# Kernel tuning notes

Measured on AMD Instinct MI355X. Metric: run time of the kernel, lower is better.

The kernel has to match this reference:

```python
import jax, jax.numpy as jnp
import numpy as np

B, N, C = 16, 2048, 256
C4 = C // 4
BN_EPS = 1e-5


def setup_inputs() -> dict:
    key = jax.random.key(0)
    ks = jax.random.split(key, 9)
    return {
        "x": jax.random.normal(ks[0], (B, N, C), jnp.float32),
        "Wq": jax.random.normal(ks[1], (C4, C), jnp.float32) * (1.0 / np.sqrt(C)),
        "Wk": jax.random.normal(ks[2], (C4, C), jnp.float32) * (1.0 / np.sqrt(C)),
        "Wv": jax.random.normal(ks[3], (C, C), jnp.float32) * (1.0 / np.sqrt(C)),
        "bv": jax.random.normal(ks[4], (C,), jnp.float32) * 0.01,
        "Wt": jax.random.normal(ks[5], (C, C), jnp.float32) * (1.0 / np.sqrt(C)),
        "bt": jax.random.normal(ks[6], (C,), jnp.float32) * 0.01,
        "gamma": jnp.ones((C,), jnp.float32),
        "beta": jnp.zeros((C,), jnp.float32),
        "bn_mean": jax.random.normal(ks[7], (C,), jnp.float32) * 0.1,
        "bn_var": jax.random.uniform(ks[8], (C,), jnp.float32, 0.5, 1.5),
    }


def reference(x, Wq, Wk, Wv, bv, Wt, bt, gamma, beta, bn_mean, bn_var):
    # x: (B, N, C) -> channel-first (B, C, N) as in the torch module
    xc = jnp.transpose(x, (0, 2, 1))                       # (B, C, N)
    q = jnp.einsum('oc,bcn->bno', Wq, xc)                  # (B, N, C4)
    k = jnp.einsum('oc,bcn->bon', Wk, xc)                  # (B, C4, N)
    # v_conv is computed in the original module but its output is never used;
    # it does not affect the forward output.
    energy = jnp.einsum('bno,bom->bnm', q, k)              # (B, N, N)
    attn = jax.nn.softmax(energy, axis=-1)
    # offset-attention double normalization: divide by column sums
    attn = attn / (1e-6 + jnp.sum(attn, axis=1, keepdims=True))
    x_r = jnp.einsum('bcn,bnm->bcm', xc, attn)             # (B, C, N)
    d = xc - x_r
    t = jnp.einsum('oc,bcn->bon', Wt, d) + bt[None, :, None]
    bn = gamma[None, :, None] * (t - bn_mean[None, :, None]) \
         * jax.lax.rsqrt(bn_var[None, :, None] + BN_EPS) + beta[None, :, None]
    out = xc + jnp.maximum(bn, 0.0)                        # residual + ReLU
    return jnp.transpose(out, (0, 2, 1))                   # (B, N, C)
```

## Files before the change

### kernel.cpp

```cpp
#include <hip/hip_runtime.h>
#include <math.h>
#include <stdint.h>

constexpr int B_ = 16, N_ = 2048, C_ = 256, K_ = 64;
constexpr float EPS_BN = 1e-5f;

typedef __attribute__((ext_vector_type(8))) short short8;
typedef __attribute__((ext_vector_type(16))) float f32x16;

#define MFMA32(A, Bf, Cc) __builtin_amdgcn_mfma_f32_32x32x16_bf16(A, Bf, Cc, 0, 0, 0)

constexpr size_t SZ_QK  = (size_t)B_*N_*K_*2;
constexpr size_t WSB_QH = 0;
constexpr size_t WSB_QL = WSB_QH + SZ_QK;
constexpr size_t WSB_KH = WSB_QL + SZ_QK;
constexpr size_t WSB_KL = WSB_KH + SZ_QK;
constexpr size_t WSB_Z  = WSB_KL + SZ_QK;
constexpr size_t WSB_CS = WSB_Z  + (size_t)B_*N_*4;
constexpr size_t WSB_WQT= WSB_CS + (size_t)B_*N_*4;
constexpr size_t WSB_WKT= WSB_WQT+ (size_t)C_*K_*4;
constexpr size_t WSB_WTT= WSB_WKT+ (size_t)C_*K_*4;
constexpr size_t WSB_S  = WSB_WTT+ (size_t)C_*C_*4;
constexpr size_t WSB_CB = WSB_S  + (size_t)C_*4;
constexpr size_t WSB_O  = (WSB_CB + (size_t)C_*4 + 255) & ~(size_t)255;

constexpr size_t XT_LO = (size_t)B_*N_*C_*2;

__device__ inline unsigned short bf16_rne(float f) {
  uint32_t u = __float_as_uint(f);
  uint32_t r = u + 0x7FFFu + ((u >> 16) & 1u);
  return (unsigned short)(r >> 16);
}

#define GLOAD_LDS16(g, l) __builtin_amdgcn_global_load_lds( \
    (const __attribute__((address_space(1))) unsigned int*)(g), \
    (__attribute__((address_space(3))) unsigned int*)(l), 16, 0, 0)

__global__ void k0_prep(const float* __restrict__ Wq, const float* __restrict__ Wk,
                        const float* __restrict__ Wt, const float* __restrict__ bt,
                        const float* __restrict__ gamma, const float* __restrict__ beta,
                        const float* __restrict__ mean, const float* __restrict__ var,
                        char* __restrict__ ws) {
  int o = blockIdx.x, c = threadIdx.x;
  ((float*)(ws + WSB_WTT))[(size_t)c*C_ + o] = Wt[(size_t)o*C_ + c];
  if (o < K_) {
    ((float*)(ws + WSB_WQT))[(size_t)c*K_ + o] = Wq[(size_t)o*C_ + c];
    ((float*)(ws + WSB_WKT))[(size_t)c*K_ + o] = Wk[(size_t)o*C_ + c];
  }
  if (o == 0) {
    float s = gamma[c] * rsqrtf(var[c] + EPS_BN);
    ((float*)(ws + WSB_S))[c]  = s;
    ((float*)(ws + WSB_CB))[c] = s * (bt[c] - mean[c]) + beta[c];
  }
}

__global__ __launch_bounds__(256) void k1_qk(const float* __restrict__ x,
                                             char* __restrict__ ws,
                                             char* __restrict__ xtbuf) {
  __shared__ float xs[32][260];
  const float* WqT = (const float*)(ws + WSB_WQT);
  const float* WkT = (const float*)(ws + WSB_WKT);
  unsigned short* qh = (unsigned short*)(ws + WSB_QH);
  unsigned short* ql = (unsigned short*)(ws + WSB_QL);
  unsigned short* kh = (unsigned short*)(ws + WSB_KH);
  unsigned short* kl = (unsigned short*)(ws + WSB_KL);
  int b = blockIdx.x >> 6, nt = blockIdx.x & 63;
  int n0 = nt * 32, tid = threadIdx.x;

  const float4* xg = (const float4*)(x + ((size_t)b*N_ + n0)*C_);
#pragma unroll
  for (int i = 0; i < 8; i++) {
    int f = tid + i*256;
    int r = f >> 6, c4 = f & 63;
    *(float4*)&xs[r][c4*4] = xg[f];
  }
  __syncthreads();

  int o = tid & 63, rg = tid >> 6;
  float aq[8], ak[8];
#pragma unroll
  for (int j = 0; j < 8; j++) { aq[j] = 0.f; ak[j] = 0.f; }
  for (int c = 0; c < C_; c++) {
    float wq = WqT[c*K_ + o];
    float wk = WkT[c*K_ + o];
#pragma unroll
    for (int j = 0; j < 8; j++) {
      float xv = xs[rg*8 + j][c];
      aq[j] = fmaf(xv, wq, aq[j]);
      ak[j] = fmaf(xv, wk, ak[j]);
    }
  }
#pragma unroll
  for (int j = 0; j < 8; j++) {
    int n = n0 + rg*8 + j;
    size_t base = ((size_t)b*N_ + n)*K_ + o;
    float q = aq[j];
    uint32_t qb = __float_as_uint(q) & 0xFFFF0000u;
    qh[base] = (unsigned short)(qb >> 16);
    ql[base] = bf16_rne(q - __uint_as_float(qb));
    float k = ak[j];
    uint32_t kb = __float_as_uint(k) & 0xFFFF0000u;
    kh[base] = (unsigned short)(kb >> 16);
    kl[base] = bf16_rne(k - __uint_as_float(kb));
  }
#pragma unroll
  for (int nc = 0; nc < 4; nc++) {
    uint32_t hw[4], lw[4];
#pragma unroll
    for (int jj = 0; jj < 4; jj++) {
      float a  = xs[nc*8 + jj*2    ][tid];
      float bv = xs[nc*8 + jj*2 + 1][tid];
      uint32_t ab = __float_as_uint(a)  & 0xFFFF0000u;
      uint32_t bb = __float_as_uint(bv) & 0xFFFF0000u;
      hw[jj] = (ab >> 16) | bb;
      float alo = a  - __uint_as_float(ab);
      float blo = bv - __uint_as_float(bb);
      lw[jj] = (uint32_t)bf16_rne(alo) | ((uint32_t)bf16_rne(blo) << 16);
    }
    size_t toff = ((size_t)(b*64 + nt))*16384 + ((size_t)nc*256 + tid)*16;
    *(uint4*)(xtbuf + toff)         = make_uint4(hw[0], hw[1], hw[2], hw[3]);
    *(uint4*)(xtbuf + XT_LO + toff) = make_uint4(lw[0], lw[1], lw[2], lw[3]);
  }
}

__global__ __launch_bounds__(256) void k3_stats(char* __restrict__ ws) {
  int b = blockIdx.x >> 4, nb = blockIdx.x & 15;
  int tid = threadIdx.x, wave = tid >> 6, l = tid & 63;
  int lo5 = l & 31, hi5 = l >> 5;
  int n = nb*128 + wave*32 + lo5;

  short8 qhf[4], qlf[4];
  size_t qoff = ((size_t)b*N_ + n)*K_;
#pragma unroll
  for (int cs = 0; cs < 4; cs++) {
    qhf[cs] = *(const short8*)(ws + WSB_QH + (qoff + cs*16 + hi5*8)*2);
    qlf[cs] = *(const short8*)(ws + WSB_QL + (qoff + cs*16 + hi5*8)*2);
  }
  float M = -3.0e38f, S = 0.f;
  for (int mt = 0; mt < 64; mt++) {
    int mm0 = mt*32;
    size_t koff = ((size_t)b*N_ + mm0 + lo5)*K_;
    short8 khf[4], klf[4];
#pragma unroll
    for (int cs = 0; cs < 4; cs++) {
      khf[cs] = *(const short8*)(ws + WSB_KH + (koff + cs*16 + hi5*8)*2);
      klf[cs] = *(const short8*)(ws + WSB_KL + (koff + cs*16 + hi5*8)*2);
    }
    f32x16 E = {0.f};
#pragma unroll
    for (int cs = 0; cs < 4; cs++) {
      E = MFMA32(khf[cs], qhf[cs], E);
      E = MFMA32(khf[cs], qlf[cs], E);
      E = MFMA32(klf[cs], qhf[cs], E);
    }
    float tmax = E[0];
#pragma unroll
    for (int r = 1; r < 16; r++) tmax = fmaxf(tmax, E[r]);
    float nM = fmaxf(M, tmax);
    float sc = __expf(M - nM);
    float ss = 0.f;
#pragma unroll
    for (int r = 0; r < 16; r++) ss += __expf(E[r] - nM);
    S = fmaf(S, sc, ss);
    M = nM;
  }
  float Mo = __shfl_xor(M, 32, 64);
  float So = __shfl_xor(S, 32, 64);
  float Mg = fmaxf(M, Mo);
  float Sg = S*__expf(M - Mg) + So*__expf(Mo - Mg);
  if (hi5 == 0)
    ((float*)(ws + WSB_Z))[(size_t)b*N_ + n] = Mg + __logf(Sg);
}

__global__ __launch_bounds__(256) void k4_ov(char* __restrict__ ws,
                                             const char* __restrict__ xtbuf) {
  __shared__ __align__(16) char xtile[32768];
  __shared__ float zs[32];
  int b = blockIdx.x >> 5, mblk = blockIdx.x & 31;
  int m0 = mblk*64;
  int tid = threadIdx.x, wave = tid >> 6, l = tid & 63;
  int lo5 = l & 31, hi5 = l >> 5;
  int msub = wave >> 1, c0 = (wave & 1)*128;
  int mg = m0 + msub*32 + lo5;

  short8 khf[4], klf[4];
  size_t koff = ((size_t)b*N_ + mg)*K_;
#pragma unroll
  for (int cs = 0; cs < 4; cs++) {
    khf[cs] = *(const short8*)(ws + WSB_KH + (koff + cs*16 + hi5*8)*2);
    klf[cs] = *(const short8*)(ws + WSB_KL + (koff + cs*16 + hi5*8)*2);
  }
  f32x16 accO[4];
#pragma unroll
  for (int ct = 0; ct < 4; ct++) accO[ct] = (f32x16){0.f};
  float csum = 0.f;
  const float* Zp = (const float*)(ws + WSB_Z);

  for (int nt = 0; nt < 64; nt++) {
    int nn0 = nt*32;
    __syncthreads();
    size_t src = (size_t)(b*64 + nt)*16384 + (size_t)tid*16;
#pragma unroll
    for (int i = 0; i < 4; i++)
      GLOAD_LDS16(xtbuf + src + (size_t)i*4096, xtile + tid*16 + i*4096);
#pragma unroll
    for (int i = 0; i < 4; i++)
      GLOAD_LDS16(xtbuf + XT_LO + src + (size_t)i*4096, xtile + 16384 + tid*16 + i*4096);
    if (tid < 32) zs[tid] = Zp[(size_t)b*N_ + nn0 + tid];
    short8 qaf[4], qalf[4];
    size_t qoff = ((size_t)b*N_ + nn0 + lo5)*K_;
#pragma unroll
    for (int cs = 0; cs < 4; cs++) {
      qaf[cs]  = *(const short8*)(ws + WSB_QH + (qoff + cs*16 + hi5*8)*2);
      qalf[cs] = *(const short8*)(ws + WSB_QL + (qoff + cs*16 + hi5*8)*2);
    }
    __syncthreads();
    f32x16 E = {0.f};
#pragma unroll
    for (int cs = 0; cs < 4; cs++) {
      E = MFMA32(qaf[cs],  khf[cs], E);
      E = MFMA32(qaf[cs],  klf[cs], E);
      E = MFMA32(qalf[cs], khf[cs], E);
    }
    float ph[16], pl[16];
#pragma unroll
    for (int r = 0; r < 16; r++) {
      int nr = (r & 3) + 8*(r >> 2) + 4*hi5;
      float p = __expf(E[r] - zs[nr]);
      csum += p;
      uint32_t pb = __float_as_uint(p) & 0xFFFF0000u;
      ph[r] = __uint_as_float(pb);
      pl[r] = p - ph[r];
    }
    uint32_t Wh[8], Wl[8];
#pragma unroll
    for (int i = 0; i < 8; i++) {
      Wh[i] = (__float_as_uint(ph[2*i]) >> 16) | (__float_as_uint(ph[2*i+1]) & 0xFFFF0000u);
      uint32_t w;
      asm("v_cvt_pk_bf16_f32 %0, %1, %2" : "=v"(w) : "v"(pl[2*i]), "v"(pl[2*i+1]));
      Wl[i] = w;
    }
    short8 pha[2], pla[2];
#pragma unroll
    for (int s = 0; s < 2; s++) {
      uint32_t a0 = Wh[s*4+0], b0 = Wh[s*4+2];
      uint32_t a1 = Wh[s*4+1], b1 = Wh[s*4+3];
      asm("v_permlane32_swap_b32 %0, %1" : "+v"(a0), "+v"(b0));
      asm("v_permlane32_swap_b32 %0, %1" : "+v"(a1), "+v"(b1));
      union { uint32_t w[4]; short8 s8; } uh;
      uh.w[0] = a0; uh.w[1] = a1; uh.w[2] = b0; uh.w[3] = b1;
      pha[s] = uh.s8;
      uint32_t c0w = Wl[s*4+0], d0 = Wl[s*4+2];
      uint32_t c1w = Wl[s*4+1], d1 = Wl[s*4+3];
      asm("v_permlane32_swap_b32 %0, %1" : "+v"(c0w), "+v"(d0));
      asm("v_permlane32_swap_b32 %0, %1" : "+v"(c1w), "+v"(d1));
      union { uint32_t w[4]; short8 s8; } ul;
      ul.w[0] = c0w; ul.w[1] = c1w; ul.w[2] = d0; ul.w[3] = d1;
      pla[s] = ul.s8;
    }
#pragma unroll
    for (int ct = 0; ct < 4; ct++) {
      int cc = c0 + ct*32 + lo5;
      short8 bh[2], bl[2];
#pragma unroll
      for (int ns = 0; ns < 2; ns++) {
        size_t off = ((size_t)((ns*2 + hi5)*256 + cc))*16;
        bh[ns] = *(const short8*)(xtile + off);
        bl[ns] = *(const short8*)(xtile + 16384 + off);
      }
#pragma unroll
      for (int ns = 0; ns < 2; ns++) {
        accO[ct] = MFMA32(pha[ns], bh[ns], accO[ct]);
        accO[ct] = MFMA32(pha[ns], bl[ns], accO[ct]);
        accO[ct] = MFMA32(pla[ns], bh[ns], accO[ct]);
      }
    }
  }
  csum += __shfl_xor(csum, 32, 64);
  if ((wave & 1) == 0 && hi5 == 0)
    ((float*)(ws + WSB_CS))[(size_t)b*N_ + mg] = csum;
  float* Op = (float*)(ws + WSB_O);
#pragma unroll
  for (int ct = 0; ct < 4; ct++) {
#pragma unroll
    for (int r = 0; r < 16; r++) {
      int mm = m0 + msub*32 + (r & 3) + 8*(r >> 2) + 4*hi5;
      int cc = c0 + ct*32 + lo5;
      Op[((size_t)b*N_ + mm)*C_ + cc] = accO[ct][r];
    }
  }
}

constexpr int BR5 = 64;
__global__ __launch_bounds__(256) void k5_epi(const float* __restrict__ x,
                                              char* __restrict__ ws,
                                              float* __restrict__ out) {
  const float* WtT  = (const float*)(ws + WSB_WTT);
  const float* Sarr = (const float*)(ws + WSB_S);
  const float* Carr = (const float*)(ws + WSB_CB);
  const float* colsum = (const float*)(ws + WSB_CS);
  const float* Oraw = (const float*)(ws + WSB_O);
  __shared__ float ds[BR5][C_];
  __shared__ float icsL[BR5];
  int b = blockIdx.x >> 5, nt = blockIdx.x & 31;
  int n0 = nt*BR5, tid = threadIdx.x;
  if (tid < BR5) icsL[tid] = 1.0f / (1e-6f + colsum[(size_t)b*N_ + n0 + tid]);
  __syncthreads();
  const float4* xg = (const float4*)(x    + ((size_t)b*N_ + n0)*C_);
  const float4* og = (const float4*)(Oraw + ((size_t)b*N_ + n0)*C_);
#pragma unroll
  for (int i = 0; i < 16; i++) {
    int f = tid + i*256;
    int r = f >> 6;
    float4 xv = xg[f];
    float4 ov = og[f];
    float ic = icsL[r];
    float4 d;
    d.x = xv.x - ov.x*ic; d.y = xv.y - ov.y*ic;
    d.z = xv.z - ov.z*ic; d.w = xv.w - ov.w*ic;
    *(float4*)&ds[r][(f & 63)*4] = d;
  }
  __syncthreads();
  int og_ = tid & 63, rg = tid >> 6;
  float acc[16][4];
#pragma unroll
  for (int r = 0; r < 16; r++)
#pragma unroll
    for (int j = 0; j < 4; j++) acc[r][j] = 0.f;
  for (int cc = 0; cc < C_; cc++) {
    float4 w = *(const float4*)&WtT[(size_t)cc*C_ + og_*4];
#pragma unroll
    for (int r = 0; r < 16; r++) {
      float dv = ds[rg*16 + r][cc];
      acc[r][0] = fmaf(dv, w.x, acc[r][0]);
      acc[r][1] = fmaf(dv, w.y, acc[r][1]);
      acc[r][2] = fmaf(dv, w.z, acc[r][2]);
      acc[r][3] = fmaf(dv, w.w, acc[r][3]);
    }
  }
  float4 s4 = *(const float4*)&Sarr[og_*4];
  float4 c4 = *(const float4*)&Carr[og_*4];
#pragma unroll
  for (int r = 0; r < 16; r++) {
    size_t row = (size_t)b*N_ + n0 + rg*16 + r;
    float4 xv = *(const float4*)&x[row*C_ + og_*4];
    float4 o;
    float bn0 = fmaf(s4.x, acc[r][0], c4.x);
    float bn1 = fmaf(s4.y, acc[r][1], c4.y);
    float bn2 = fmaf(s4.z, acc[r][2], c4.z);
    float bn3 = fmaf(s4.w, acc[r][3], c4.w);
    o.x = xv.x + (bn0 > 0.f ? bn0 : 0.f);
    o.y = xv.y + (bn1 > 0.f ? bn1 : 0.f);
    o.z = xv.z + (bn2 > 0.f ? bn2 : 0.f);
    o.w = xv.w + (bn3 > 0.f ? bn3 : 0.f);
    *(float4*)&out[row*C_ + og_*4] = o;
  }
}

extern "C" void kernel_launch(void* const* d_in, const int* in_sizes, int n_in,
                              void* d_out, int out_size, void* d_ws, size_t ws_size,
                              hipStream_t stream) {
  (void)in_sizes; (void)n_in; (void)out_size; (void)ws_size;
  const float* x     = (const float*)d_in[0];
  const float* Wq    = (const float*)d_in[1];
  const float* Wk    = (const float*)d_in[2];
  const float* Wt    = (const float*)d_in[5];
  const float* bt    = (const float*)d_in[6];
  const float* gamma = (const float*)d_in[7];
  const float* beta  = (const float*)d_in[8];
  const float* mean  = (const float*)d_in[9];
  const float* var   = (const float*)d_in[10];
  char* ws = (char*)d_ws;
  char* xt = (char*)d_out;
  float* out = (float*)d_out;

  k0_prep <<<C_,        C_,  0, stream>>>(Wq, Wk, Wt, bt, gamma, beta, mean, var, ws);
  k1_qk   <<<B_*64,     256, 0, stream>>>(x, ws, xt);
  k3_stats<<<B_*16,     256, 0, stream>>>(ws);
  k4_ov   <<<B_*32,     256, 0, stream>>>(ws, xt);
  k5_epi  <<<B_*32,     256, 0, stream>>>(x, ws, out);
}
```

Baseline: 451.6 us.

## Fuse epilogue transform GEMM into attention kernel with double-buffered LDS staging

Merges the separate epilogue kernel into the attention-output kernel. Each block now normalises its output by the column sums, forms d = x - x_r in a swizzled LDS tile, and runs the Wt projection with split-bf16 MFMA before applying BN, ReLU and the residual. This removes the round trip of the raw O tensor and colsum through global memory, and moves the epilogue from scalar FMA loops onto MFMA. It also double-buffers the x-tile and Q loads across iterations to overlap loads with compute. The trade-off is doubled LDS use (64KB) and more register pressure, which may limit occupancy.

```diff
diff --git a/kernel.cpp b/kernel.cpp
--- a/kernel.cpp
+++ b/kernel.cpp
@@ -16,15 +16,14 @@
 constexpr size_t WSB_KH = WSB_QL + SZ_QK;
 constexpr size_t WSB_KL = WSB_KH + SZ_QK;
 constexpr size_t WSB_Z  = WSB_KL + SZ_QK;
-constexpr size_t WSB_CS = WSB_Z  + (size_t)B_*N_*4;
-constexpr size_t WSB_WQT= WSB_CS + (size_t)B_*N_*4;
+constexpr size_t WSB_WQT= WSB_Z  + (size_t)B_*N_*4;
 constexpr size_t WSB_WKT= WSB_WQT+ (size_t)C_*K_*4;
-constexpr size_t WSB_WTT= WSB_WKT+ (size_t)C_*K_*4;
-constexpr size_t WSB_S  = WSB_WTT+ (size_t)C_*C_*4;
+constexpr size_t WSB_S  = WSB_WKT+ (size_t)C_*K_*4;
 constexpr size_t WSB_CB = WSB_S  + (size_t)C_*4;
-constexpr size_t WSB_O  = (WSB_CB + (size_t)C_*4 + 255) & ~(size_t)255;
-
-constexpr size_t XT_LO = (size_t)B_*N_*C_*2;
+constexpr size_t WSB_WBH= WSB_CB + (size_t)C_*4;
+constexpr size_t WSB_WBL= WSB_WBH+ (size_t)C_*C_*2;
+constexpr size_t WSB_XT = (WSB_WBL + (size_t)C_*C_*2 + 255) & ~(size_t)255;
+constexpr size_t XT_HALF= (size_t)B_*N_*C_*2;
 
 __device__ inline unsigned short bf16_rne(float f) {
   uint32_t u = __float_as_uint(f);
@@ -42,7 +41,12 @@
                         const float* __restrict__ mean, const float* __restrict__ var,
                         char* __restrict__ ws) {
   int o = blockIdx.x, c = threadIdx.x;
-  ((float*)(ws + WSB_WTT))[(size_t)c*C_ + o] = Wt[(size_t)o*C_ + c];
+  {
+    float w = Wt[(size_t)o*C_ + c];
+    uint32_t wb = __float_as_uint(w) & 0xFFFF0000u;
+    ((unsigned short*)(ws + WSB_WBH))[(size_t)o*C_ + c] = (unsigned short)(wb >> 16);
+    ((unsigned short*)(ws + WSB_WBL))[(size_t)o*C_ + c] = bf16_rne(w - __uint_as_float(wb));
+  }
   if (o < K_) {
     ((float*)(ws + WSB_WQT))[(size_t)c*K_ + o] = Wq[(size_t)o*C_ + c];
     ((float*)(ws + WSB_WKT))[(size_t)c*K_ + o] = Wk[(size_t)o*C_ + c];
@@ -118,8 +122,8 @@
       lw[jj] = (uint32_t)bf16_rne(alo) | ((uint32_t)bf16_rne(blo) << 16);
     }
     size_t toff = ((size_t)(b*64 + nt))*16384 + ((size_t)nc*256 + tid)*16;
-    *(uint4*)(xtbuf + toff)         = make_uint4(hw[0], hw[1], hw[2], hw[3]);
-    *(uint4*)(xtbuf + XT_LO + toff) = make_uint4(lw[0], lw[1], lw[2], lw[3]);
+    *(uint4*)(xtbuf + toff)           = make_uint4(hw[0], hw[1], hw[2], hw[3]);
+    *(uint4*)(xtbuf + XT_HALF + toff) = make_uint4(lw[0], lw[1], lw[2], lw[3]);
   }
 }
 
@@ -138,8 +142,7 @@
   }
   float M = -3.0e38f, S = 0.f;
   for (int mt = 0; mt < 64; mt++) {
-    int mm0 = mt*32;
-    size_t koff = ((size_t)b*N_ + mm0 + lo5)*K_;
+    size_t koff = ((size_t)b*N_ + mt*32 + lo5)*K_;
     short8 khf[4], klf[4];
 #pragma unroll
     for (int cs = 0; cs < 4; cs++) {
@@ -172,16 +175,21 @@
     ((float*)(ws + WSB_Z))[(size_t)b*N_ + n] = Mg + __logf(Sg);
 }
 
-__global__ __launch_bounds__(256) void k4_ov(char* __restrict__ ws,
-                                             const char* __restrict__ xtbuf) {
-  __shared__ __align__(16) char xtile[32768];
-  __shared__ float zs[32];
+__global__ __launch_bounds__(256, 2) void k4_ov(const float* __restrict__ x,
+                                                char* __restrict__ ws,
+                                                float* __restrict__ out) {
+  __shared__ __align__(16) char xtile[65536];
+  __shared__ float zsb[2][32];
+  __shared__ float csL[64];
   int b = blockIdx.x >> 5, mblk = blockIdx.x & 31;
   int m0 = mblk*64;
   int tid = threadIdx.x, wave = tid >> 6, l = tid & 63;
   int lo5 = l & 31, hi5 = l >> 5;
   int msub = wave >> 1, c0 = (wave & 1)*128;
   int mg = m0 + msub*32 + lo5;
+  const float* Zp = (const float*)(ws + WSB_Z);
+  const char* XTH = ws + WSB_XT;
+  const char* XTL = ws + WSB_XT + XT_HALF;
 
   short8 khf[4], klf[4];
   size_t koff = ((size_t)b*N_ + mg)*K_;
@@ -194,39 +202,37 @@
 #pragma unroll
   for (int ct = 0; ct < 4; ct++) accO[ct] = (f32x16){0.f};
   float csum = 0.f;
-  const float* Zp = (const float*)(ws + WSB_Z);
-
-  for (int nt = 0; nt < 64; nt++) {
-    int nn0 = nt*32;
-    __syncthreads();
+
+  auto STAGE = [&](int nt, int buf) {
     size_t src = (size_t)(b*64 + nt)*16384 + (size_t)tid*16;
-#pragma unroll
-    for (int i = 0; i < 4; i++)
-      GLOAD_LDS16(xtbuf + src + (size_t)i*4096, xtile + tid*16 + i*4096);
-#pragma unroll
-    for (int i = 0; i < 4; i++)
-      GLOAD_LDS16(xtbuf + XT_LO + src + (size_t)i*4096, xtile + 16384 + tid*16 + i*4096);
-    if (tid < 32) zs[tid] = Zp[(size_t)b*N_ + nn0 + tid];
-    short8 qaf[4], qalf[4];
-    size_t qoff = ((size_t)b*N_ + nn0 + lo5)*K_;
+    char* dst = xtile + buf*32768 + tid*16;
+#pragma unroll
+    for (int i = 0; i < 4; i++) GLOAD_LDS16(XTH + src + (size_t)i*4096, dst + i*4096);
+#pragma unroll
+    for (int i = 0; i < 4; i++) GLOAD_LDS16(XTL + src + (size_t)i*4096, dst + 16384 + i*4096);
+    if (tid < 32) zsb[buf][tid] = Zp[(size_t)b*N_ + nt*32 + tid];
+  };
+  auto QLOAD = [&](int nt, short8* qh8, short8* ql8) {
+    size_t qoff2 = ((size_t)b*N_ + nt*32 + lo5)*K_;
 #pragma unroll
     for (int cs = 0; cs < 4; cs++) {
-      qaf[cs]  = *(const short8*)(ws + WSB_QH + (qoff + cs*16 + hi5*8)*2);
-      qalf[cs] = *(const short8*)(ws + WSB_QL + (qoff + cs*16 + hi5*8)*2);
-    }
-    __syncthreads();
+      qh8[cs] = *(const short8*)(ws + WSB_QH + (qoff2 + cs*16 + hi5*8)*2);
+      ql8[cs] = *(const short8*)(ws + WSB_QL + (qoff2 + cs*16 + hi5*8)*2);
+    }
+  };
+  auto COMPUTE = [&](int buf, const short8* qh8, const short8* ql8) {
     f32x16 E = {0.f};
 #pragma unroll
     for (int cs = 0; cs < 4; cs++) {
-      E = MFMA32(qaf[cs],  khf[cs], E);
-      E = MFMA32(qaf[cs],  klf[cs], E);
-      E = MFMA32(qalf[cs], khf[cs], E);
+      E = MFMA32(qh8[cs], khf[cs], E);
+      E = MFMA32(qh8[cs], klf[cs], E);
+      E = MFMA32(ql8[cs], khf[cs], E);
     }
     float ph[16], pl[16];
 #pragma unroll
     for (int r = 0; r < 16; r++) {
       int nr = (r & 3) + 8*(r >> 2) + 4*hi5;
-      float p = __expf(E[r] - zs[nr]);
+      float p = __expf(E[r] - zsb[buf][nr]);
       csum += p;
       uint32_t pb = __float_as_uint(p) & 0xFFFF0000u;
       ph[r] = __uint_as_float(pb);
@@ -258,6 +264,7 @@
       ul.w[0] = c0w; ul.w[1] = c1w; ul.w[2] = d0; ul.w[3] = d1;
       pla[s] = ul.s8;
     }
+    const char* xb = xtile + buf*32768;
 #pragma unroll
     for (int ct = 0; ct < 4; ct++) {
       int cc = c0 + ct*32 + lo5;
@@ -265,8 +272,8 @@
 #pragma unroll
       for (int ns = 0; ns < 2; ns++) {
         size_t off = ((size_t)((ns*2 + hi5)*256 + cc))*16;
-        bh[ns] = *(const short8*)(xtile + off);
-        bl[ns] = *(const short8*)(xtile + 16384 + off);
+        bh[ns] = *(const short8*)(xb + off);
+        bl[ns] = *(const short8*)(xb + 16384 + off);
       }
 #pragma unroll
       for (int ns = 0; ns < 2; ns++) {
@@ -275,86 +282,89 @@
         accO[ct] = MFMA32(pla[ns], bh[ns], accO[ct]);
       }
     }
-  }
+  };
+
+  short8 qA[4], qlA[4], qB[4], qlB[4];
+  STAGE(0, 0); QLOAD(0, qA, qlA);
+  __syncthreads();
+  for (int base = 0; base < 64; base += 2) {
+    STAGE(base + 1, 1); QLOAD(base + 1, qB, qlB);
+    COMPUTE(0, qA, qlA);
+    __syncthreads();
+    if (base + 2 < 64) { STAGE(base + 2, 0); QLOAD(base + 2, qA, qlA); }
+    COMPUTE(1, qB, qlB);
+    __syncthreads();
+  }
+
   csum += __shfl_xor(csum, 32, 64);
-  if ((wave & 1) == 0 && hi5 == 0)
-    ((float*)(ws + WSB_CS))[(size_t)b*N_ + mg] = csum;
-  float* Op = (float*)(ws + WSB_O);
-#pragma unroll
-  for (int ct = 0; ct < 4; ct++) {
-#pragma unroll
-    for (int r = 0; r < 16; r++) {
-      int mm = m0 + msub*32 + (r & 3) + 8*(r >> 2) + 4*hi5;
+  if ((wave & 1) == 0 && hi5 == 0) csL[msub*32 + lo5] = csum;
+  __syncthreads();
+#pragma unroll
+  for (int r = 0; r < 16; r++) {
+    int mloc = msub*32 + (r & 3) + 8*(r >> 2) + 4*hi5;
+    float ics = 1.0f / (1e-6f + csL[mloc]);
+#pragma unroll
+    for (int ct = 0; ct < 4; ct++) {
       int cc = c0 + ct*32 + lo5;
-      Op[((size_t)b*N_ + mm)*C_ + cc] = accO[ct][r];
-    }
-  }
-}
-
-constexpr int BR5 = 64;
-__global__ __launch_bounds__(256) void k5_epi(const float* __restrict__ x,
-                                              char* __restrict__ ws,
-                                              float* __restrict__ out) {
-  const float* WtT  = (const float*)(ws + WSB_WTT);
-  const float* Sarr = (const float*)(ws + WSB_S);
-  const float* Carr = (const float*)(ws + WSB_CB);
-  const float* colsum = (const float*)(ws + WSB_CS);
-  const float* Oraw = (const float*)(ws + WSB_O);
-  __shared__ float ds[BR5][C_];
-  __shared__ float icsL[BR5];
-  int b = blockIdx.x >> 5, nt = blockIdx.x & 31;
-  int n0 = nt*BR5, tid = threadIdx.x;
-  if (tid < BR5) icsL[tid] = 1.0f / (1e-6f + colsum[(size_t)b*N_ + n0 + tid]);
+      float xv = x[((size_t)b*N_ + m0 + mloc)*C_ + cc];
+      float dv = fmaf(-accO[ct][r], ics, xv);
+      uint32_t db = __float_as_uint(dv) & 0xFFFF0000u;
+      int byte = mloc*512 + ((((cc >> 3) ^ (mloc & 31)) << 4)) + ((cc & 7) << 1);
+      *(unsigned short*)(xtile + byte)         = (unsigned short)(db >> 16);
+      *(unsigned short*)(xtile + 32768 + byte) = bf16_rne(dv - __uint_as_float(db));
+    }
+  }
   __syncthreads();
-  const float4* xg = (const float4*)(x    + ((size_t)b*N_ + n0)*C_);
-  const float4* og = (const float4*)(Oraw + ((size_t)b*N_ + n0)*C_);
-#pragma unroll
-  for (int i = 0; i < 16; i++) {
-    int f = tid + i*256;
-    int r = f >> 6;
-    float4 xv = xg[f];
-    float4 ov = og[f];
-    float ic = icsL[r];
-    float4 d;
-    d.x = xv.x - ov.x*ic; d.y = xv.y - ov.y*ic;
-    d.z = xv.z - ov.z*ic; d.w = xv.w - ov.w*ic;
-    *(float4*)&ds[r][(f & 63)*4] = d;
-  }
-  __syncthreads();
-  int og_ = tid & 63, rg = tid >> 6;
-  float acc[16][4];
-#pragma unroll
-  for (int r = 0; r < 16; r++)
-#pragma unroll
-    for (int j = 0; j < 4; j++) acc[r][j] = 0.f;
-  for (int cc = 0; cc < C_; cc++) {
-    float4 w = *(const float4*)&WtT[(size_t)cc*C_ + og_*4];
-#pragma unroll
-    for (int r = 0; r < 16; r++) {
-      float dv = ds[rg*16 + r][cc];
-      acc[r][0] = fmaf(dv, w.x, acc[r][0]);
-      acc[r][1] = fmaf(dv, w.y, acc[r][1]);
-      acc[r][2] = fmaf(dv, w.z, acc[r][2]);
-      acc[r][3] = fmaf(dv, w.w, acc[r][3]);
-    }
-  }
-  float4 s4 = *(const float4*)&Sarr[og_*4];
-  float4 c4 = *(const float4*)&Carr[og_*4];
-#pragma unroll
-  for (int r = 0; r < 16; r++) {
-    size_t row = (size_t)b*N_ + n0 + rg*16 + r;
-    float4 xv = *(const float4*)&x[row*C_ + og_*4];
-    float4 o;
-    float bn0 = fmaf(s4.x, acc[r][0], c4.x);
-    float bn1 = fmaf(s4.y, acc[r][1], c4.y);
-    float bn2 = fmaf(s4.z, acc[r][2], c4.z);
-    float bn3 = fmaf(s4.w, acc[r][3], c4.w);
-    o.x = xv.x + (bn0 > 0.f ? bn0 : 0.f);
-    o.y = xv.y + (bn1 > 0.f ? bn1 : 0.f);
-    o.z = xv.z + (bn2 > 0.f ? bn2 : 0.f);
-    o.w = xv.w + (bn3 > 0.f ? bn3 : 0.f);
-    *(float4*)&out[row*C_ + og_*4] = o;
-  }
+  f32x16 accT[2][2];
+#pragma unroll
+  for (int ms = 0; ms < 2; ms++)
+#pragma unroll
+    for (int ot = 0; ot < 2; ot++) accT[ms][ot] = (f32x16){0.f};
+#pragma unroll
+  for (int cs = 0; cs < 16; cs++) {
+    short8 ah[2], al[2], bh[2], bl[2];
+#pragma unroll
+    for (int ms = 0; ms < 2; ms++) {
+      int off = (ms*32 + lo5)*512 + ((((cs*2 + hi5) ^ lo5)) << 4);
+      ah[ms] = *(const short8*)(xtile + off);
+      al[ms] = *(const short8*)(xtile + 32768 + off);
+    }
+#pragma unroll
+    for (int ot = 0; ot < 2; ot++) {
+      size_t wo = ((size_t)((wave*2 + ot)*32 + lo5)*C_ + cs*16 + hi5*8)*2;
+      bh[ot] = *(const short8*)(ws + WSB_WBH + wo);
+      bl[ot] = *(const short8*)(ws + WSB_WBL + wo);
+    }
+#pragma unroll
+    for (int ms = 0; ms < 2; ms++)
+#pragma unroll
+      for (int ot = 0; ot < 2; ot++) {
+        accT[ms][ot] = MFMA32(ah[ms], bh[ot], accT[ms][ot]);
+        accT[ms][ot] = MFMA32(ah[ms], bl[ot], accT[ms][ot]);
+        accT[ms][ot] = MFMA32(al[ms], bh[ot], accT[ms][ot]);
+      }
+  }
+  const float* Sp = (const float*)(ws + WSB_S);
+  const float* Cp = (const float*)(ws + WSB_CB);
+  float sv[2], cv[2];
+#pragma unroll
+  for (int ot = 0; ot < 2; ot++) {
+    int o = (wave*2 + ot)*32 + lo5;
+    sv[ot] = Sp[o]; cv[ot] = Cp[o];
+  }
+#pragma unroll
+  for (int ms = 0; ms < 2; ms++)
+#pragma unroll
+    for (int ot = 0; ot < 2; ot++)
+#pragma unroll
+      for (int r = 0; r < 16; r++) {
+        int mloc = ms*32 + (r & 3) + 8*(r >> 2) + 4*hi5;
+        int o = (wave*2 + ot)*32 + lo5;
+        float bn = fmaf(sv[ot], accT[ms][ot][r], cv[ot]);
+        bn = bn > 0.f ? bn : 0.f;
+        size_t idx = ((size_t)b*N_ + m0 + mloc)*C_ + o;
+        out[idx] = x[idx] + bn;
+      }
 }
 
 extern "C" void kernel_launch(void* const* d_in, const int* in_sizes, int n_in,
@@ -371,12 +381,10 @@
   const float* mean  = (const float*)d_in[9];
   const float* var   = (const float*)d_in[10];
   char* ws = (char*)d_ws;
-  char* xt = (char*)d_out;
   float* out = (float*)d_out;
 
-  k0_prep <<<C_,        C_,  0, stream>>>(Wq, Wk, Wt, bt, gamma, beta, mean, var, ws);
-  k1_qk   <<<B_*64,     256, 0, stream>>>(x, ws, xt);
-  k3_stats<<<B_*16,     256, 0, stream>>>(ws);
-  k4_ov   <<<B_*32,     256, 0, stream>>>(ws, xt);
-  k5_epi  <<<B_*32,     256, 0, stream>>>(x, ws, out);
-}
+  k0_prep <<<C_,     C_,  0, stream>>>(Wq, Wk, Wt, bt, gamma, beta, mean, var, ws);
+  k1_qk   <<<B_*64,  256, 0, stream>>>(x, ws, ws + WSB_XT);
+  k3_stats<<<B_*16,  256, 0, stream>>>(ws);
+  k4_ov   <<<B_*32,  256, 0, stream>>>(x, ws, out);
+}
```

New measurement: 413.8 us. -8.4%, faster.
